# Kernel optimization log

Hardware: AMD Instinct MI355X
Metric: run time of the kernel (lower is better)

Reference implementation:

```python
import jax, jax.numpy as jnp
from jax import lax
import numpy as np

FEA = 256
NHEADS = 8
GROUPS = 32
SCALE = 1.0 / np.sqrt(FEA // NHEADS)  # 1/sqrt(qkv_dim//nheads)


def conv2d(x, w, b=None, pad=0, groups=1):
    out = lax.conv_general_dilated(
        x, w, (1, 1), [(pad, pad), (pad, pad)],
        dimension_numbers=("NCHW", "OIHW", "NCHW"),
        feature_group_count=groups)
    return out if b is None else out + b[None, :, None, None]


def group_norm(x, w, b, groups=GROUPS, eps=1e-5):
    B, C, H, W = x.shape
    xg = x.reshape(B, groups, C // groups, H, W)
    m = xg.mean(axis=(2, 3, 4), keepdims=True)
    v = xg.var(axis=(2, 3, 4), keepdims=True)
    xg = (xg - m) * lax.rsqrt(v + eps)
    return xg.reshape(B, C, H, W) * w[None, :, None, None] + b[None, :, None, None]


def l2norm(x, eps=1e-12):  # F.normalize over channel dim
    n = jnp.sqrt(jnp.sum(x * x, axis=1, keepdims=True))
    return x / jnp.maximum(n, eps)


def attn_op(q, k, v):
    b, c, xf, yf = q.shape
    sp = lambda t: t.reshape(b, NHEADS, c // NHEADS, xf * yf)
    q, k, v = sp(q), sp(k), sp(v)
    sim = jnp.einsum("bhjn,bhkn->bhjk", q, k) * SCALE  # channel attention, [b,h,c/h,c/h]
    sim = jax.nn.softmax(sim, axis=-1)
    out = jnp.einsum("bhjk,bhkn->bhjn", sim, v)
    return out.reshape(b, c, xf, yf)


def freqca(x, gn_w, gn_b, dw_w, pw_w, pw_b, ao_w, ao_b, f1_w, f2_w, f3_w, f3_b):
    H, W = x.shape[-2:]
    x = group_norm(x, gn_w, gn_b)
    qkv = conv2d(conv2d(x, dw_w, pad=1, groups=FEA), pw_w, pw_b)  # depthwise 3x3 then 1x1 -> 3*qkv_dim
    q, k, v = jnp.split(qkv, 3, axis=1)
    q, k, v = l2norm(q), l2norm(k), l2norm(v)
    qf = jnp.fft.rfft2(q, axes=(-2, -1), norm="ortho")
    kf = jnp.fft.rfft2(k, axes=(-2, -1), norm="ortho")
    vf = jnp.fft.rfft2(v, axes=(-2, -1), norm="ortho")
    amp = attn_op(jnp.abs(qf), jnp.abs(kf), jnp.abs(vf))
    phas = attn_op(jnp.angle(qf), jnp.angle(kf), jnp.angle(vf))
    out_c = amp * jnp.cos(phas) + 1j * (amp * jnp.sin(phas))  # torch.polar
    out = jnp.fft.irfft2(out_c, s=(H, W), axes=(-2, -1), norm="ortho")
    attn = conv2d(out, ao_w, ao_b) + x  # attn_res is Identity (fea_dim == dim_out)
    h = jax.nn.silu(conv2d(attn, f1_w, pad=1))
    h = conv2d(h, f2_w, pad=1)
    h = conv2d(h, f3_w, f3_b)
    return h + attn  # DropPath in eval mode = identity


def setup_inputs() -> dict:
    key = jax.random.key(0)
    ks = jax.random.split(key, 12)
    B, C, H, W = 8, FEA, 128, 128
    s = 0.02
    return {
        "x": jax.random.normal(ks[0], (B, C, H, W), jnp.float32),
        "gn_w": jnp.ones((C,), jnp.float32),
        "gn_b": jnp.zeros((C,), jnp.float32),
        "dw_w": jax.random.normal(ks[1], (C, 1, 3, 3), jnp.float32) * s,
        "pw_w": jax.random.normal(ks[2], (3 * C, C, 1, 1), jnp.float32) * s,
        "pw_b": jnp.zeros((3 * C,), jnp.float32),
        "ao_w": jax.random.normal(ks[3], (C, C, 1, 1), jnp.float32) * s,
        "ao_b": jnp.zeros((C,), jnp.float32),
        "f1_w": jax.random.normal(ks[4], (2 * C, C, 3, 3), jnp.float32) * s,
        "f2_w": jax.random.normal(ks[5], (C, 2 * C, 3, 3), jnp.float32) * s,
        "f3_w": jax.random.normal(ks[6], (C, C, 1, 1), jnp.float32) * s,
        "f3_b": jnp.zeros((C,), jnp.float32),
    }


def reference(x, gn_w, gn_b, dw_w, pw_w, pw_b, ao_w, ao_b, f1_w, f2_w, f3_w, f3_b):
    return freqca(x, gn_w, gn_b, dw_w, pw_w, pw_b, ao_w, ao_b, f1_w, f2_w, f3_w, f3_b)
```

## Files before the change

kernel.cpp:

```cpp
#include <hip/hip_runtime.h>
#include <hip/hip_bf16.h>
#include <math.h>


#define TWO_PI_D 6.283185307179586476925286766559
#define ATTN_SCALE 0.17677669529663687f

typedef __attribute__((ext_vector_type(8))) short short8;
typedef __attribute__((ext_vector_type(4))) short short4v;
typedef __attribute__((ext_vector_type(4))) float f32x4;
typedef _Float16 half8v __attribute__((ext_vector_type(8)));

__device__ inline short f2bf(float f) {
    __hip_bfloat16 h = __float2bfloat16(f);
    return *reinterpret_cast<short*>(&h);
}
__device__ inline unsigned short h_bits(_Float16 h) {
    union { _Float16 h; unsigned short u; } c; c.h = h; return c.u;
}

__global__ __launch_bounds__(256) void groupnorm_kernel(
    const float* __restrict__ x, const float* __restrict__ gw,
    const float* __restrict__ gb, float* __restrict__ out, int b0)
{
    int t = threadIdx.x;
    int lb = blockIdx.x >> 5;
    int g  = blockIdx.x & 31;
    size_t src = ((size_t)(b0 + lb) * 32 + g) * 131072;
    size_t dst = (size_t)blockIdx.x * 131072;
    const float* xp = x + src;
    double s = 0.0, ss = 0.0;
    for (int i = t; i < 131072; i += 256) { double v = xp[i]; s += v; ss += v*v; }
    __shared__ double rs[256], rss[256];
    rs[t] = s; rss[t] = ss;
    __syncthreads();
    for (int k = 128; k > 0; k >>= 1) {
        if (t < k) { rs[t] += rs[t+k]; rss[t] += rss[t+k]; }
        __syncthreads();
    }
    __shared__ float smean, sinv;
    if (t == 0) {
        double mean = rs[0] * (1.0/131072.0);
        double var  = rss[0] * (1.0/131072.0) - mean*mean;
        smean = (float)mean;
        sinv  = (float)(1.0 / sqrt(var + 1e-5));
    }
    __syncthreads();
    float mean = smean, inv = sinv;
    for (int i = t; i < 131072; i += 256) {
        int c = (g << 3) + (i >> 14);
        out[dst + i] = (xp[i] - mean) * inv * gw[c] + gb[c];
    }
}

__global__ __launch_bounds__(256) void dwconv_kernel(
    const float* __restrict__ in, const float* __restrict__ w, float* __restrict__ out)
{
    int t = threadIdx.x;
    int bc = blockIdx.x >> 6;
    int y  = ((blockIdx.x & 63) << 1) + (t >> 7);
    int x  = t & 127;
    int c  = bc & 255;
    const float* wp = w + c*9;
    const float* ip = in + ((size_t)bc << 14);
    float acc = 0.f;
    #pragma unroll
    for (int dy = 0; dy < 3; dy++) {
        int yy = y + dy - 1;
        if (yy < 0 || yy > 127) continue;
        const float* row = ip + (yy << 7);
        #pragma unroll
        for (int dx = 0; dx < 3; dx++) {
            int xx = x + dx - 1;
            if (xx >= 0 && xx <= 127) acc += wp[dy*3+dx] * row[xx];
        }
    }
    out[((size_t)bc << 14) + (y << 7) + x] = acc;
}

__global__ __launch_bounds__(256) void wcvtpw_kernel(
    const float* __restrict__ w, _Float16* __restrict__ whi,
    _Float16* __restrict__ wlo, int total)
{
    int i = blockIdx.x * 256 + threadIdx.x;
    if (i >= total) return;
    float v = w[i];
    _Float16 h = (_Float16)v;
    _Float16 l = (_Float16)(v - (float)h);
    whi[i] = h; wlo[i] = l;
}

__global__ __launch_bounds__(256) void twcvt_kernel(
    _Float16* __restrict__ twh, _Float16* __restrict__ twl)
{
    int i = blockIdx.x * 256 + threadIdx.x;
    if (i >= 20480) return;
    int bin = i >> 7, w = i & 127;
    double v = 0.0;
    if (bin < 65) v = cos(TWO_PI_D * ((bin * w) & 127) / 128.0) * 0.0078125;
    else if (bin < 130) v = -sin(TWO_PI_D * (((bin - 65) * w) & 127) / 128.0) * 0.0078125;
    _Float16 h = (_Float16)v;
    twh[i] = h;
    twl[i] = (_Float16)((float)v - (float)h);
}

__global__ __launch_bounds__(256) void convpw_kernel(
    const float* __restrict__ in, const _Float16* __restrict__ whi,
    const _Float16* __restrict__ wlo, const float* __restrict__ bias,
    float* __restrict__ out)
{
    int y      = blockIdx.x;
    int coBase = blockIdx.y << 7;
    int lb     = blockIdx.z;
    int t = threadIdx.x;
    int lane = t & 63;
    int wave = t >> 6;
    int wm = (wave >> 1) << 6;
    int wn = (wave & 1) << 6;
    int lr = lane & 15;
    int kg = (lane >> 4) << 3;

    __shared__ _Float16 Ah[128][40], Al[128][40];
    __shared__ _Float16 Bh[128][40], Bl[128][40];

    f32x4 acc[4][4];
    #pragma unroll
    for (int i = 0; i < 4; i++)
        #pragma unroll
        for (int j = 0; j < 4; j++) acc[i][j] = (f32x4){0.f, 0.f, 0.f, 0.f};

    const float* inrow = in + (((size_t)lb * 256) << 14) + (y << 7);
    for (int ci0 = 0; ci0 < 256; ci0 += 32) {
        __syncthreads();
        #pragma unroll
        for (int u = 0; u < 2; u++) {
            int ii = t + (u << 8);
            int co = ii >> 2, cg = ii & 3;
            *(half8v*)&Ah[co][cg << 3] =
                *(const half8v*)&whi[(size_t)(coBase + co) * 256 + ci0 + (cg << 3)];
            *(half8v*)&Al[co][cg << 3] =
                *(const half8v*)&wlo[(size_t)(coBase + co) * 256 + ci0 + (cg << 3)];
        }
        for (int i = t; i < 2048; i += 256) {
            int px = i & 127, chp = i >> 7;
            int ci = ci0 + (chp << 1);
            float v0 = inrow[((size_t)ci << 14) + px];
            float v1 = inrow[((size_t)(ci + 1) << 14) + px];
            _Float16 h0 = (_Float16)v0, h1 = (_Float16)v1;
            _Float16 l0 = (_Float16)(v0 - (float)h0);
            _Float16 l1 = (_Float16)(v1 - (float)h1);
            unsigned uh = (unsigned)h_bits(h0) | ((unsigned)h_bits(h1) << 16);
            unsigned ul = (unsigned)h_bits(l0) | ((unsigned)h_bits(l1) << 16);
            *(unsigned*)&Bh[px][chp << 1] = uh;
            *(unsigned*)&Bl[px][chp << 1] = ul;
        }
        __syncthreads();
        half8v ah[4], al[4], bh4[4], bl4[4];
        #pragma unroll
        for (int i = 0; i < 4; i++) {
            ah[i] = *(const half8v*)&Ah[wm + i*16 + lr][kg];
            al[i] = *(const half8v*)&Al[wm + i*16 + lr][kg];
        }
        #pragma unroll
        for (int j = 0; j < 4; j++) {
            bh4[j] = *(const half8v*)&Bh[wn + j*16 + lr][kg];
            bl4[j] = *(const half8v*)&Bl[wn + j*16 + lr][kg];
        }
        #pragma unroll
        for (int i = 0; i < 4; i++)
            #pragma unroll
            for (int j = 0; j < 4; j++) {
                acc[i][j] = __builtin_amdgcn_mfma_f32_16x16x32_f16(
                    ah[i], bh4[j], acc[i][j], 0, 0, 0);
                acc[i][j] = __builtin_amdgcn_mfma_f32_16x16x32_f16(
                    ah[i], bl4[j], acc[i][j], 0, 0, 0);
                acc[i][j] = __builtin_amdgcn_mfma_f32_16x16x32_f16(
                    al[i], bh4[j], acc[i][j], 0, 0, 0);
            }
    }

    int pBase = y << 7;
    int mr = (lane >> 4) << 2;
    #pragma unroll
    for (int i = 0; i < 4; i++) {
        int co0 = coBase + wm + i*16 + mr;
        #pragma unroll
        for (int j = 0; j < 4; j++) {
            int px = pBase + wn + j*16 + lr;
            #pragma unroll
            for (int r = 0; r < 4; r++) {
                out[(((size_t)(lb*768 + co0 + r)) << 14) + px] =
                    acc[i][j][r] + bias[co0 + r];
            }
        }
    }
}

__global__ __launch_bounds__(256) void l2inv_kernel(
    const float* __restrict__ qkv, float* __restrict__ invn)
{
    int p  = ((blockIdx.x & 63) << 8) + threadIdx.x;
    int bT = blockIdx.x >> 6;
    int lb = bT / 3, T = bT - 3*lb;
    const float* base = qkv + (((size_t)(lb*768 + T*256)) << 14) + p;
    double ss = 0.0;
    for (int c = 0; c < 256; c++) { double v = base[(size_t)c << 14]; ss += v*v; }
    invn[((size_t)bT << 14) + p] = 1.f / fmaxf((float)sqrt(ss), 1e-12f);
}

__global__ __launch_bounds__(256) void fftrow_mfma_kernel(
    const float* __restrict__ qkv, const float* __restrict__ invn,
    const _Float16* __restrict__ twh, const _Float16* __restrict__ twl,
    float* __restrict__ rre, float* __restrict__ rim, int chunkBase)
{
    int loc = blockIdx.x;
    int gp  = chunkBase + loc;
    int t = threadIdx.x;
    int lane = t & 63;
    int wave = t >> 6;
    int wm  = (wave >> 1) << 6;
    int wnn = (wave & 1) * 80;
    int lr = lane & 15;
    int kq = (lane >> 4) << 3;

    __shared__ _Float16 Xh[128][68], Xl[128][68];

    int lb = gp / 768, chn = gp - lb*768, T = chn >> 8;
    const float4* src = (const float4*)(qkv + ((size_t)gp << 14));
    const float4* ivp = (const float4*)(invn + (((size_t)(lb*3 + T)) << 14));

    f32x4 acc[4][5];
    #pragma unroll
    for (int i = 0; i < 4; i++)
        #pragma unroll
        for (int j = 0; j < 5; j++) acc[i][j] = (f32x4){0.f, 0.f, 0.f, 0.f};

    for (int half = 0; half < 2; half++) {
        __syncthreads();
        for (int i = t; i < 2048; i += 256) {
            int r = i >> 4, q4 = i & 15;
            int gi = (r << 5) + (half << 4) + q4;
            float4 v = src[gi], w = ivp[gi];
            v.x *= w.x; v.y *= w.y; v.z *= w.z; v.w *= w.w;
            int cl = q4 << 2;
            _Float16 h0 = (_Float16)v.x, h1 = (_Float16)v.y;
            _Float16 h2 = (_Float16)v.z, h3 = (_Float16)v.w;
            Xh[r][cl+0] = h0; Xh[r][cl+1] = h1; Xh[r][cl+2] = h2; Xh[r][cl+3] = h3;
            Xl[r][cl+0] = (_Float16)(v.x - (float)h0);
            Xl[r][cl+1] = (_Float16)(v.y - (float)h1);
            Xl[r][cl+2] = (_Float16)(v.z - (float)h2);
            Xl[r][cl+3] = (_Float16)(v.w - (float)h3);
        }
        __syncthreads();
        #pragma unroll
        for (int ks = 0; ks < 2; ks++) {
            int k0 = (ks << 5) + kq;
            int kg = (half << 6) + k0;
            half8v ah[4], al[4], bh[5], bl[5];
            #pragma unroll
            for (int i = 0; i < 4; i++) {
                ah[i] = *(const half8v*)&Xh[wm + i*16 + lr][k0];
                al[i] = *(const half8v*)&Xl[wm + i*16 + lr][k0];
            }
            #pragma unroll
            for (int j = 0; j < 5; j++) {
                int bin = wnn + j*16 + lr;
                bh[j] = *(const half8v*)&twh[(size_t)bin * 128 + kg];
                bl[j] = *(const half8v*)&twl[(size_t)bin * 128 + kg];
            }
            #pragma unroll
            for (int i = 0; i < 4; i++)
                #pragma unroll
                for (int j = 0; j < 5; j++) {
                    acc[i][j] = __builtin_amdgcn_mfma_f32_16x16x32_f16(
                        ah[i], bh[j], acc[i][j], 0, 0, 0);
                    acc[i][j] = __builtin_amdgcn_mfma_f32_16x16x32_f16(
                        al[i], bh[j], acc[i][j], 0, 0, 0);
                    acc[i][j] = __builtin_amdgcn_mfma_f32_16x16x32_f16(
                        ah[i], bl[j], acc[i][j], 0, 0, 0);
                }
        }
    }

    int mr = (lane >> 4) << 2;
    #pragma unroll
    for (int i = 0; i < 4; i++) {
        #pragma unroll
        for (int j = 0; j < 5; j++) {
            int bin = wnn + j*16 + lr;
            if (bin < 130) {
                float* dst = (bin < 65) ? rre : rim;
                int bb = (bin < 65) ? bin : bin - 65;
                #pragma unroll
                for (int r = 0; r < 4; r++) {
                    int row = wm + i*16 + mr + r;
                    dst[((size_t)loc*128 + row)*65 + bb] = acc[i][j][r];
                }
            }
        }
    }
}

__global__ __launch_bounds__(256) void fft_col_kernel(
    const float* __restrict__ rre, const float* __restrict__ rim,
    float* __restrict__ spec, int chunkBase, size_t slotStride)
{
    int kb  = blockIdx.x * 13;
    int loc = blockIdx.y;
    int gp  = chunkBase + loc;
    int t   = threadIdx.x;
    __shared__ float zr[128][14], zi[128][14];
    __shared__ float gr[8][16][14], gi[8][16][14];
    __shared__ float ct[128], st[128];
    if (t < 128) { double s, c; sincos(TWO_PI_D * t / 128.0, &s, &c);
                   st[t] = (float)s; ct[t] = (float)c; }
    for (int i = t; i < 1664; i += 256) {
        int r = i / 13, k = i - r*13;
        size_t si = ((size_t)loc*128 + r)*65 + kb + k;
        zr[r][k] = rre[si];
        zi[r][k] = rim[si];
    }
    __syncthreads();
    for (int i = t; i < 1664; i += 256) {
        int kx = i % 13, rm = i / 13;
        int r0 = rm >> 4, m = rm & 15;
        int step = (m << 3) & 127;
        float gre = 0.f, gim = 0.f;
        int idx = 0;
        for (int r1 = 0; r1 < 16; r1++) {
            float cc = ct[idx], sn = st[idx];
            float a = zr[(r1 << 3) + r0][kx], b = zi[(r1 << 3) + r0][kx];
            gre += a*cc + b*sn;
            gim += b*cc - a*sn;
            idx = (idx + step) & 127;
        }
        gr[r0][m][kx] = gre;
        gi[r0][m][kx] = gim;
    }
    __syncthreads();
    int lb = gp / 768; int chn = gp - lb*768;
    int T = chn >> 8;  int c = chn & 255;
    float* aD = spec + (size_t)(2*T)   * slotStride + ((size_t)(lb*256 + c))*8320;
    float* pD = spec + (size_t)(2*T+1) * slotStride + ((size_t)(lb*256 + c))*8320;
    for (int i = t; i < 1664; i += 256) {
        int kx = i % 13, k1 = i / 13;
        int m = k1 & 15;
        float re = 0.f, im = 0.f;
        int idx = 0;
        for (int r0 = 0; r0 < 8; r0++) {
            float cc = ct[idx], sn = st[idx];
            float a = gr[r0][m][kx], b = gi[r0][m][kx];
            re += a*cc + b*sn;
            im += b*cc - a*sn;
            idx = (idx + k1) & 127;
        }
        int kxv = kb + kx;
        if ((k1 == 0 || k1 == 64) && (kxv == 0 || kxv == 64)) im = 0.f;
        int oi = k1*65 + kxv;
        aD[oi] = sqrtf(re*re + im*im);
        pD[oi] = atan2f(im, re);
    }
}

__global__ __launch_bounds__(256) void attn_sim_kernel(
    const float* __restrict__ qA, const float* __restrict__ kA,
    float* __restrict__ simpart)
{
    int sp = blockIdx.x;
    int bh = blockIdx.y;
    int lb = bh >> 3, h = bh & 7;
    int t = threadIdx.x;
    __shared__ float qs[32][132], ks[32][132];
    const float* qb = qA + ((size_t)(lb*256 + h*32)) * 8320;
    const float* kb = kA + ((size_t)(lb*256 + h*32)) * 8320;
    float acc[4] = {0.f, 0.f, 0.f, 0.f};
    int j0 = t >> 5;
    int kq = t & 31;
    for (int sub = 0; sub < 4; sub++) {
        int n0 = sp*520 + sub*130;
        __syncthreads();
        for (int i = t; i < 4160; i += 256) {
            int j = i / 130, nn = i - j*130;
            qs[j][nn] = qb[(size_t)j*8320 + n0 + nn];
            ks[j][nn] = kb[(size_t)j*8320 + n0 + nn];
        }
        __syncthreads();
        for (int nn = 0; nn < 128; nn += 4) {
            float4 kv = *(const float4*)&ks[kq][nn];
            #pragma unroll
            for (int e = 0; e < 4; e++) {
                float4 qv = *(const float4*)&qs[j0 + e*8][nn];
                acc[e] += qv.x*kv.x + qv.y*kv.y + qv.z*kv.z + qv.w*kv.w;
            }
        }
        {
            float2 kv = *(const float2*)&ks[kq][128];
            #pragma unroll
            for (int e = 0; e < 4; e++) {
                float2 qv = *(const float2*)&qs[j0 + e*8][128];
                acc[e] += qv.x*kv.x + qv.y*kv.y;
            }
        }
    }
    float* dst = simpart + ((size_t)bh*16 + sp) * 1024;
    dst[t]       = acc[0];
    dst[t + 256] = acc[1];
    dst[t + 512] = acc[2];
    dst[t + 768] = acc[3];
}

__global__ __launch_bounds__(256) void attn_out_kernel(
    const float* __restrict__ simpart, const float* __restrict__ vA,
    float* __restrict__ outA)
{
    int nb = blockIdx.x << 8;
    int bh = blockIdx.y;
    int lb = bh >> 3, h = bh & 7;
    int t = threadIdx.x;
    __shared__ float sim[32][32];
    for (int e = t; e < 1024; e += 256) {
        float s = 0.f;
        const float* pp = simpart + (size_t)bh*16384 + e;
        #pragma unroll
        for (int sp = 0; sp < 16; sp++) s += pp[sp*1024];
        sim[e >> 5][e & 31] = s * ATTN_SCALE;
    }
    __syncthreads();
    if (t < 32) {
        float m = -1e30f;
        for (int k = 0; k < 32; k++) m = fmaxf(m, sim[t][k]);
        float s = 0.f;
        for (int k = 0; k < 32; k++) s += expf(sim[t][k] - m);
        float inv = 1.f / s;
        for (int k = 0; k < 32; k++) sim[t][k] = expf(sim[t][k] - m) * inv;
    }
    __syncthreads();
    int n = nb + t;
    if (n >= 8320) return;
    const float* vb = vA + ((size_t)(lb*256 + h*32)) * 8320 + n;
    float vv[32];
    #pragma unroll
    for (int k = 0; k < 32; k++) vv[k] = vb[(size_t)k * 8320];
    float* ob = outA + ((size_t)(lb*256 + h*32)) * 8320 + n;
    for (int j = 0; j < 32; j++) {
        float o = 0.f;
        #pragma unroll
        for (int k = 0; k < 32; k++) o += sim[j][k] * vv[k];
        ob[(size_t)j * 8320] = o;
    }
}

__global__ __launch_bounds__(256) void ifft_col_kernel(
    const float* __restrict__ ampo, const float* __restrict__ pho,
    float* __restrict__ tre, float* __restrict__ tim)
{
    int kb    = blockIdx.x * 13;
    int plane = blockIdx.y;
    int t     = threadIdx.x;
    __shared__ float zr[128][14], zi[128][14];
    __shared__ float gr[8][16][14], gi[8][16][14];
    __shared__ float ct[128], st[128];
    if (t < 128) { double s, c; sincos(TWO_PI_D * t / 128.0, &s, &c);
                   st[t] = (float)s; ct[t] = (float)c; }
    const float* ab = ampo + (size_t)plane * 8320;
    const float* pb = pho  + (size_t)plane * 8320;
    for (int i = t; i < 1664; i += 256) {
        int k1 = i / 13, k = i - k1*13;
        float a = ab[k1*65 + kb + k];
        float p = pb[k1*65 + kb + k];
        float sp, cp; sincosf(p, &sp, &cp);
        zr[k1][k] = a * cp;
        zi[k1][k] = a * sp;
    }
    __syncthreads();
    for (int i = t; i < 1664; i += 256) {
        int kx = i % 13, rm = i / 13;
        int r0 = rm >> 4, m = rm & 15;
        int step = (m << 3) & 127;
        float gre = 0.f, gim = 0.f;
        int idx = 0;
        for (int r1 = 0; r1 < 16; r1++) {
            float cc = ct[idx], sn = st[idx];
            float a = zr[(r1 << 3) + r0][kx], b = zi[(r1 << 3) + r0][kx];
            gre += a*cc - b*sn;
            gim += a*sn + b*cc;
            idx = (idx + step) & 127;
        }
        gr[r0][m][kx] = gre;
        gi[r0][m][kx] = gim;
    }
    __syncthreads();
    for (int i = t; i < 1664; i += 256) {
        int kx = i % 13, y = i / 13;
        int m = y & 15;
        float re = 0.f, im = 0.f;
        int idx = 0;
        for (int r0 = 0; r0 < 8; r0++) {
            float cc = ct[idx], sn = st[idx];
            float a = gr[r0][m][kx], b = gi[r0][m][kx];
            re += a*cc - b*sn;
            im += a*sn + b*cc;
            idx = (idx + y) & 127;
        }
        size_t oi = ((size_t)plane*128 + y)*65 + kb + kx;
        tre[oi] = re;
        tim[oi] = im;
    }
}

__global__ __launch_bounds__(256) void ifft_row_kernel(
    const float* __restrict__ tre, const float* __restrict__ tim,
    float* __restrict__ spat)
{
    int rc    = blockIdx.x;
    int plane = blockIdx.y;
    int t     = threadIdx.x;
    __shared__ float tr[16][66], ti[16][66];
    __shared__ float ct[128], st[128];
    if (t < 128) { double s, c; sincos(TWO_PI_D * t / 128.0, &s, &c);
                   st[t] = (float)s; ct[t] = (float)c; }
    for (int i = t; i < 1040; i += 256) {
        int r = i / 65, k = i - r*65;
        size_t si = ((size_t)plane*128 + rc*16 + r)*65 + k;
        float sc = (k >= 1 && k < 64) ? 2.f : 1.f;
        tr[r][k] = tre[si] * sc;
        ti[r][k] = tim[si] * sc;
    }
    __syncthreads();
    for (int oo = t; oo < 260; oo += 256) {
        int x = oo % 65, rq = oo / 65;
        int r0i = rq << 2;
        float C0 = tr[r0i+0][0], C1 = tr[r0i+1][0], C2 = tr[r0i+2][0], C3 = tr[r0i+3][0];
        float S0 = 0.f, S1 = 0.f, S2 = 0.f, S3 = 0.f;
        int m = x;
        for (int k = 1; k <= 64; k++) {
            float cc = ct[m], sn = st[m];
            C0 += tr[r0i+0][k]*cc; S0 += ti[r0i+0][k]*sn;
            C1 += tr[r0i+1][k]*cc; S1 += ti[r0i+1][k]*sn;
            C2 += tr[r0i+2][k]*cc; S2 += ti[r0i+2][k]*sn;
            C3 += tr[r0i+3][k]*cc; S3 += ti[r0i+3][k]*sn;
            m = (m + x) & 127;
        }
        size_t ob = ((size_t)plane << 14) + ((rc*16 + r0i) << 7);
        spat[ob + x]       = (C0 - S0)*0.0078125f;
        spat[ob + 128 + x] = (C1 - S1)*0.0078125f;
        spat[ob + 256 + x] = (C2 - S2)*0.0078125f;
        spat[ob + 384 + x] = (C3 - S3)*0.0078125f;
        if (x >= 1 && x <= 63) {
            int xm = 128 - x;
            spat[ob + xm]       = (C0 + S0)*0.0078125f;
            spat[ob + 128 + xm] = (C1 + S1)*0.0078125f;
            spat[ob + 256 + xm] = (C2 + S2)*0.0078125f;
            spat[ob + 384 + xm] = (C3 + S3)*0.0078125f;
        }
    }
}

__global__ __launch_bounds__(256) void wcvt_kernel(
    const float* __restrict__ w, short* __restrict__ wbf,
    int Cout, int Cin, int RR)
{
    int i = blockIdx.x * 256 + threadIdx.x;
    int total = Cout * Cin * RR;
    if (i >= total) return;
    int rr = i % RR;
    int ci = (i / RR) % Cin;
    int co = i / (RR * Cin);
    wbf[((size_t)rr * Cout + co) * Cin + ci] = f2bf(w[i]);
}

__global__ __launch_bounds__(256) void convmf2_kernel(
    const float* __restrict__ in, const short* __restrict__ wbf,
    const float* __restrict__ bias, const float* __restrict__ res,
    float* __restrict__ out, short* __restrict__ out_t,
    int Cin, int Cout, int act, int in_b0, int res_b0, int out_b0)
{
    int y      = blockIdx.x;
    int coBase = blockIdx.y << 7;
    int lb = blockIdx.z;
    int t = threadIdx.x;
    int lane = t & 63;
    int wave = t >> 6;
    int wm = (wave >> 1) << 6;
    int wn = (wave & 1) << 6;

    __shared__ short As[128][40];
    __shared__ short Bs[128][40];

    f32x4 acc[4][4];
    #pragma unroll
    for (int i = 0; i < 4; i++)
        #pragma unroll
        for (int j = 0; j < 4; j++) acc[i][j] = (f32x4){0.f, 0.f, 0.f, 0.f};

    const size_t inb = ((size_t)(in_b0 + lb) * Cin) << 14;
    int lr = lane & 15;
    int kg = (lane >> 4) << 3;

    const float* inrow = in + inb + (y << 7);
    const short* wslice = wbf + (size_t)coBase * Cin;
    for (int ci0 = 0; ci0 < Cin; ci0 += 32) {
        __syncthreads();
        #pragma unroll
        for (int u = 0; u < 2; u++) {
            int ii = t + (u << 8);
            int co = ii >> 2, cg = ii & 3;
            *(short8*)&As[co][cg << 3] =
                *(const short8*)&wslice[(size_t)co * Cin + ci0 + (cg << 3)];
        }
        for (int i = t; i < 2048; i += 256) {
            int px = i & 127, chp = i >> 7;
            int ci = ci0 + (chp << 1);
            float v0 = inrow[((size_t)ci << 14) + px];
            float v1 = inrow[((size_t)(ci + 1) << 14) + px];
            unsigned u2 = (unsigned)(unsigned short)f2bf(v0)
                        | ((unsigned)(unsigned short)f2bf(v1) << 16);
            *(unsigned*)&Bs[px][chp << 1] = u2;
        }
        __syncthreads();
        short8 af[4], bf[4];
        #pragma unroll
        for (int i = 0; i < 4; i++)
            af[i] = *(const short8*)&As[wm + i*16 + lr][kg];
        #pragma unroll
        for (int j = 0; j < 4; j++)
            bf[j] = *(const short8*)&Bs[wn + j*16 + lr][kg];
        #pragma unroll
        for (int i = 0; i < 4; i++)
            #pragma unroll
            for (int j = 0; j < 4; j++)
                acc[i][j] = __builtin_amdgcn_mfma_f32_16x16x32_bf16(
                    af[i], bf[j], acc[i][j], 0, 0, 0);
    }

    int pBase = y << 7;
    int mr = (lane >> 4) << 2;
    #pragma unroll
    for (int i = 0; i < 4; i++) {
        int co0 = coBase + wm + i*16 + mr;
        #pragma unroll
        for (int j = 0; j < 4; j++) {
            int px = pBase + wn + j*16 + lr;
            float v[4];
            #pragma unroll
            for (int r = 0; r < 4; r++) {
                float vv = acc[i][j][r] + (bias ? bias[co0 + r] : 0.f);
                if (act == 1) vv = vv / (1.f + expf(-vv));
                if (res) vv += res[(((size_t)(res_b0 + lb) * Cout + co0 + r) << 14) + px];
                v[r] = vv;
            }
            if (out) {
                #pragma unroll
                for (int r = 0; r < 4; r++)
                    out[(((size_t)(out_b0 + lb) * Cout + co0 + r) << 14) + px] = v[r];
            }
            if (out_t) {
                short4v s4 = { f2bf(v[0]), f2bf(v[1]), f2bf(v[2]), f2bf(v[3]) };
                *(short4v*)&out_t[((size_t)(lb*16384 + px)) * Cout + co0] = s4;
            }
        }
    }
}

template<int R>
__global__ __launch_bounds__(256) void convmf3_kernel(
    const short* __restrict__ in_t, const short* __restrict__ wbf,
    const float* __restrict__ bias, const float* __restrict__ res,
    float* __restrict__ out, short* __restrict__ out_t,
    int Cin, int Cout, int act, int res_b0, int out_b0)
{
    int y      = blockIdx.x;
    int coBase = blockIdx.y << 7;
    int lb = blockIdx.z;
    int t = threadIdx.x;
    int lane = t & 63;
    int wave = t >> 6;
    int wm = (wave >> 1) << 6;
    int wn = (wave & 1) << 6;
    int lr = lane & 15;
    int kg = (lane >> 4) << 3;

    f32x4 acc[4][4];
    #pragma unroll
    for (int i = 0; i < 4; i++)
        #pragma unroll
        for (int j = 0; j < 4; j++) acc[i][j] = (f32x4){0.f, 0.f, 0.f, 0.f};

    const short* inb = in_t + (((size_t)lb << 14)) * Cin;
    const short8 zero8 = {0,0,0,0,0,0,0,0};

    for (int rr = 0; rr < R*R; rr++) {
        int dy = (R == 3) ? (rr / 3) : 0;
        int dx = (R == 3) ? (rr - dy*3) : 0;
        int yy = (R == 3) ? (y + dy - 1) : y;
        if (R == 3 && (yy < 0 || yy > 127)) continue;
        const short* wsl  = wbf + ((size_t)rr * Cout + coBase) * Cin;
        const short* brow = inb + ((size_t)(yy << 7)) * Cin;
        for (int ci0 = 0; ci0 < Cin; ci0 += 32) {
            short8 af[4], bf[4];
            #pragma unroll
            for (int i = 0; i < 4; i++)
                af[i] = *(const short8*)&wsl[(size_t)(wm + i*16 + lr) * Cin + ci0 + kg];
            #pragma unroll
            for (int j = 0; j < 4; j++) {
                int pxl = wn + j*16 + lr;
                int xx = (R == 3) ? (pxl + dx - 1) : pxl;
                if (R == 3 && (xx < 0 || xx > 127)) bf[j] = zero8;
                else bf[j] = *(const short8*)&brow[(size_t)xx * Cin + ci0 + kg];
            }
            #pragma unroll
            for (int i = 0; i < 4; i++)
                #pragma unroll
                for (int j = 0; j < 4; j++)
                    acc[i][j] = __builtin_amdgcn_mfma_f32_16x16x32_bf16(
                        af[i], bf[j], acc[i][j], 0, 0, 0);
        }
    }

    int pBase = y << 7;
    int mr = (lane >> 4) << 2;
    #pragma unroll
    for (int i = 0; i < 4; i++) {
        int co0 = coBase + wm + i*16 + mr;
        #pragma unroll
        for (int j = 0; j < 4; j++) {
            int px = pBase + wn + j*16 + lr;
            float v[4];
            #pragma unroll
            for (int r = 0; r < 4; r++) {
                float vv = acc[i][j][r] + (bias ? bias[co0 + r] : 0.f);
                if (act == 1) vv = vv / (1.f + expf(-vv));
                if (res) vv += res[(((size_t)(res_b0 + lb) * Cout + co0 + r) << 14) + px];
                v[r] = vv;
            }
            if (out) {
                #pragma unroll
                for (int r = 0; r < 4; r++)
                    out[(((size_t)(out_b0 + lb) * Cout + co0 + r) << 14) + px] = v[r];
            }
            if (out_t) {
                short4v s4 = { f2bf(v[0]), f2bf(v[1]), f2bf(v[2]), f2bf(v[3]) };
                *(short4v*)&out_t[((size_t)(lb*16384 + px)) * Cout + co0] = s4;
            }
        }
    }
}

extern "C" void kernel_launch(void* const* d_in, const int* in_sizes, int n_in,
                              void* d_out, int out_size, void* d_ws, size_t ws_size,
                              hipStream_t stream) {
    (void)in_sizes; (void)n_in; (void)out_size;
    const float* x    = (const float*)d_in[0];
    const float* gn_w = (const float*)d_in[1];
    const float* gn_b = (const float*)d_in[2];
    const float* dw_w = (const float*)d_in[3];
    const float* pw_w = (const float*)d_in[4];
    const float* pw_b = (const float*)d_in[5];
    const float* ao_w = (const float*)d_in[6];
    const float* ao_b = (const float*)d_in[7];
    const float* f1_w = (const float*)d_in[8];
    const float* f2_w = (const float*)d_in[9];
    const float* f3_w = (const float*)d_in[10];
    const float* f3_b = (const float*)d_in[11];
    float* outp = (float*)d_out;

    const size_t F_QKV  = 12582912;
    const size_t F_SLOT = 2129920;
    const size_t F_SPEC = 6 * F_SLOT;
    const size_t F_XN   = 4194304;
    const size_t F_E    = 4259840;
    const size_t F_SIMP = 262144;
    const size_t F_TOT  = F_QKV + F_SPEC + F_XN + F_E + F_SIMP;
    const size_t F_WB   = 1462272;

    int NB = 0;
    for (int cand : {8, 4, 2, 1}) {
        if (((size_t)cand * F_TOT + F_WB) * 4 <= ws_size) { NB = cand; break; }
    }
    if (NB == 0) return;

    float* wsf  = (float*)d_ws;
    float* qkv  = wsf;
    short* abuf = (short*)wsf;
    short* h1t  = (short*)(wsf + (size_t)NB * 2097152);
    short* h2t  = (short*)(wsf + (size_t)NB * 6291456);
    float* spec = wsf + (size_t)NB * F_QKV;
    size_t ss   = (size_t)NB * F_SLOT;
    float* tre  = spec + 2*ss;
    float* tim  = spec + 3*ss;
    float* spat = spec + 4*ss;
    float* xn   = spec + 6*ss;
    float* ebuf = xn + (size_t)NB * F_XN;
    float* dw   = ebuf;
    float* rre  = ebuf;
    float* rim  = ebuf + (size_t)NB * 2129920;
    float* simpf = ebuf + (size_t)NB * F_E;
    float* invn  = simpf;
    float* simp  = simpf;
    short* wb    = (short*)(wsf + (size_t)NB * F_TOT);
    short* wb_ao = wb;
    short* wb_f1 = wb + 65536;
    short* wb_f2 = wb + 1245184;
    short* wb_f3 = wb + 2424832;
    _Float16* wb_pw_hi = (_Float16*)(wb + 2490368);
    _Float16* wb_pw_lo = (_Float16*)(wb + 2686976);
    _Float16* wb_tw_hi = (_Float16*)(wb + 2883584);
    _Float16* wb_tw_lo = (_Float16*)(wb + 2904064);

    wcvt_kernel<<<256,  256, 0, stream>>>(ao_w, wb_ao, 256, 256, 1);
    wcvt_kernel<<<4608, 256, 0, stream>>>(f1_w, wb_f1, 512, 256, 9);
    wcvt_kernel<<<4608, 256, 0, stream>>>(f2_w, wb_f2, 256, 512, 9);
    wcvt_kernel<<<256,  256, 0, stream>>>(f3_w, wb_f3, 256, 256, 1);
    wcvtpw_kernel<<<768, 256, 0, stream>>>(pw_w, wb_pw_hi, wb_pw_lo, 196608);
    twcvt_kernel<<<80, 256, 0, stream>>>(wb_tw_hi, wb_tw_lo);

    const int passes = 8 / NB;
    for (int p = 0; p < passes; p++) {
        int b0 = p * NB;
        groupnorm_kernel<<<NB*32, 256, 0, stream>>>(x, gn_w, gn_b, xn, b0);
        dwconv_kernel<<<NB*256*64, 256, 0, stream>>>(xn, dw_w, dw);
        convpw_kernel<<<dim3(128, 6, NB), 256, 0, stream>>>(
            dw, wb_pw_hi, wb_pw_lo, pw_b, qkv);
        l2inv_kernel<<<NB*3*64, 256, 0, stream>>>(qkv, invn);
        for (int chunk = 0; chunk < 3; chunk++) {
            fftrow_mfma_kernel<<<NB*256, 256, 0, stream>>>(
                qkv, invn, wb_tw_hi, wb_tw_lo, rre, rim, chunk*NB*256);
            fft_col_kernel<<<dim3(5, NB*256), 256, 0, stream>>>(
                rre, rim, spec, chunk*NB*256, ss);
        }
        attn_sim_kernel<<<dim3(16, NB*8), 256, 0, stream>>>(spec + 0*ss, spec + 2*ss, simp);
        attn_out_kernel<<<dim3(33, NB*8), 256, 0, stream>>>(simp, spec + 4*ss, spec + 0*ss);
        attn_sim_kernel<<<dim3(16, NB*8), 256, 0, stream>>>(spec + 1*ss, spec + 3*ss, simp);
        attn_out_kernel<<<dim3(33, NB*8), 256, 0, stream>>>(simp, spec + 5*ss, spec + 1*ss);
        ifft_col_kernel<<<dim3(5, NB*256), 256, 0, stream>>>(spec + 0*ss, spec + 1*ss,
                                                             tre, tim);
        ifft_row_kernel<<<dim3(8, NB*256), 256, 0, stream>>>(tre, tim, spat);
        convmf2_kernel<<<dim3(128, 2, NB), 256, 0, stream>>>(
            spat, wb_ao, ao_b, xn, outp, abuf, 256, 256, 0, 0, 0, b0);
        convmf3_kernel<3><<<dim3(128, 4, NB), 256, 0, stream>>>(
            abuf, wb_f1, nullptr, nullptr, nullptr, h1t, 256, 512, 1, 0, 0);
        convmf3_kernel<3><<<dim3(128, 2, NB), 256, 0, stream>>>(
            h1t, wb_f2, nullptr, nullptr, nullptr, h2t, 512, 256, 0, 0, 0);
        convmf3_kernel<1><<<dim3(128, 2, NB), 256, 0, stream>>>(
            h2t, wb_f3, f3_b, outp, outp, nullptr, 256, 256, 0, b0, b0);
    }
}
```

Baseline: 6.460 ms.

## Replace inverse column FFT with split-fp16 MFMA DFT matmul; tile dwconv rows in LDS

The inverse FFT along the column axis is recast as a dense complex DFT matrix multiply (a 256x256 real-expanded twiddle matrix) executed with fp16 MFMA using hi/lo splitting for near-fp32 accuracy, replacing the scalar radix-16x8 shared-memory DFT. A new precompute kernel builds the twiddle matrix once. The depthwise conv now stages its four input rows in shared memory to avoid redundant global loads. The MFMA path does more raw flops than an FFT and relies on three-term split precision, trading arithmetic count for matrix-core throughput.

```diff
diff --git a/kernel.cpp b/kernel.cpp
--- a/kernel.cpp
+++ b/kernel.cpp
@@ -58,24 +58,30 @@
 {
     int t = threadIdx.x;
     int bc = blockIdx.x >> 6;
-    int y  = ((blockIdx.x & 63) << 1) + (t >> 7);
-    int x  = t & 127;
+    int ystrip = (blockIdx.x & 63) << 1;
     int c  = bc & 255;
     const float* wp = w + c*9;
     const float* ip = in + ((size_t)bc << 14);
+    __shared__ float xs[4][128];
+    for (int i = t; i < 512; i += 256) {
+        int rr = i >> 7, xx = i & 127;
+        int yy = ystrip - 1 + rr;
+        xs[rr][xx] = (yy >= 0 && yy < 128) ? ip[(yy << 7) + xx] : 0.f;
+    }
+    __syncthreads();
+    int r0 = t >> 7;
+    int x  = t & 127;
     float acc = 0.f;
     #pragma unroll
     for (int dy = 0; dy < 3; dy++) {
-        int yy = y + dy - 1;
-        if (yy < 0 || yy > 127) continue;
-        const float* row = ip + (yy << 7);
+        const float* row = xs[r0 + dy];
         #pragma unroll
         for (int dx = 0; dx < 3; dx++) {
             int xx = x + dx - 1;
             if (xx >= 0 && xx <= 127) acc += wp[dy*3+dx] * row[xx];
         }
     }
-    out[((size_t)bc << 14) + (y << 7) + x] = acc;
+    out[((size_t)bc << 14) + ((ystrip + r0) << 7) + x] = acc;
 }
 
 __global__ __launch_bounds__(256) void wcvtpw_kernel(
@@ -102,6 +108,24 @@
     _Float16 h = (_Float16)v;
     twh[i] = h;
     twl[i] = (_Float16)((float)v - (float)h);
+}
+
+__global__ __launch_bounds__(256) void micvt_kernel(
+    _Float16* __restrict__ mih, _Float16* __restrict__ mil)
+{
+    int i = blockIdx.x * 256 + threadIdx.x;
+    if (i >= 65536) return;
+    int row = i >> 8, col = i & 255;
+    int k1 = col >> 1, u = col & 1;
+    int yy = row & 127;
+    double ang = TWO_PI_D * ((k1 * yy) & 127) / 128.0;
+    double cc = cos(ang), sn = sin(ang);
+    double v;
+    if (row < 128) v = (u == 0) ? cc : -sn;
+    else           v = (u == 0) ? sn :  cc;
+    _Float16 h = (_Float16)v;
+    mih[i] = h;
+    mil[i] = (_Float16)((float)v - (float)h);
 }
 
 __global__ __launch_bounds__(256) void convpw_kernel(
@@ -450,61 +474,95 @@
     }
 }
 
-__global__ __launch_bounds__(256) void ifft_col_kernel(
+__global__ __launch_bounds__(256) void ifftcol_mfma_kernel(
     const float* __restrict__ ampo, const float* __restrict__ pho,
+    const _Float16* __restrict__ mih, const _Float16* __restrict__ mil,
     float* __restrict__ tre, float* __restrict__ tim)
 {
-    int kb    = blockIdx.x * 13;
-    int plane = blockIdx.y;
-    int t     = threadIdx.x;
-    __shared__ float zr[128][14], zi[128][14];
-    __shared__ float gr[8][16][14], gi[8][16][14];
-    __shared__ float ct[128], st[128];
-    if (t < 128) { double s, c; sincos(TWO_PI_D * t / 128.0, &s, &c);
-                   st[t] = (float)s; ct[t] = (float)c; }
+    int plane = blockIdx.x;
+    int t = threadIdx.x;
+    int lane = t & 63;
+    int wave = t >> 6;
+    int wm = wave << 6;
+    int lr = lane & 15;
+    int kg = (lane >> 4) << 3;
+
+    __shared__ _Float16 Bh[80][72], Bl[80][72];
+
     const float* ab = ampo + (size_t)plane * 8320;
     const float* pb = pho  + (size_t)plane * 8320;
-    for (int i = t; i < 1664; i += 256) {
-        int k1 = i / 13, k = i - k1*13;
-        float a = ab[k1*65 + kb + k];
-        float p = pb[k1*65 + kb + k];
-        float sp, cp; sincosf(p, &sp, &cp);
-        zr[k1][k] = a * cp;
-        zi[k1][k] = a * sp;
-    }
-    __syncthreads();
-    for (int i = t; i < 1664; i += 256) {
-        int kx = i % 13, rm = i / 13;
-        int r0 = rm >> 4, m = rm & 15;
-        int step = (m << 3) & 127;
-        float gre = 0.f, gim = 0.f;
-        int idx = 0;
-        for (int r1 = 0; r1 < 16; r1++) {
-            float cc = ct[idx], sn = st[idx];
-            float a = zr[(r1 << 3) + r0][kx], b = zi[(r1 << 3) + r0][kx];
-            gre += a*cc - b*sn;
-            gim += a*sn + b*cc;
-            idx = (idx + step) & 127;
-        }
-        gr[r0][m][kx] = gre;
-        gi[r0][m][kx] = gim;
-    }
-    __syncthreads();
-    for (int i = t; i < 1664; i += 256) {
-        int kx = i % 13, y = i / 13;
-        int m = y & 15;
-        float re = 0.f, im = 0.f;
-        int idx = 0;
-        for (int r0 = 0; r0 < 8; r0++) {
-            float cc = ct[idx], sn = st[idx];
-            float a = gr[r0][m][kx], b = gi[r0][m][kx];
-            re += a*cc - b*sn;
-            im += a*sn + b*cc;
-            idx = (idx + y) & 127;
-        }
-        size_t oi = ((size_t)plane*128 + y)*65 + kb + kx;
-        tre[oi] = re;
-        tim[oi] = im;
+
+    f32x4 acc[4][5];
+    #pragma unroll
+    for (int i = 0; i < 4; i++)
+        #pragma unroll
+        for (int j = 0; j < 5; j++) acc[i][j] = (f32x4){0.f, 0.f, 0.f, 0.f};
+
+    for (int kc = 0; kc < 4; kc++) {
+        __syncthreads();
+        for (int i = t; i < 2080; i += 256) {
+            int k1l = i / 65, kx = i - k1l*65;
+            int k1 = (kc << 5) + k1l;
+            float a = ab[k1*65 + kx];
+            float p = pb[k1*65 + kx];
+            float sp, cp; sincosf(p, &sp, &cp);
+            float zr = a * cp, zi = a * sp;
+            _Float16 hr = (_Float16)zr, hi = (_Float16)zi;
+            unsigned uh = (unsigned)h_bits(hr) | ((unsigned)h_bits(hi) << 16);
+            unsigned ul = (unsigned)h_bits((_Float16)(zr - (float)hr))
+                        | ((unsigned)h_bits((_Float16)(zi - (float)hi)) << 16);
+            *(unsigned*)&Bh[kx][k1l << 1] = uh;
+            *(unsigned*)&Bl[kx][k1l << 1] = ul;
+        }
+        __syncthreads();
+        #pragma unroll
+        for (int ks = 0; ks < 2; ks++) {
+            int kq = (ks << 5) + kg;
+            int kgl = (kc << 6) + kq;
+            half8v ah[4], al[4], bh[5], bl[5];
+            #pragma unroll
+            for (int i = 0; i < 4; i++) {
+                int row = wm + i*16 + lr;
+                ah[i] = *(const half8v*)&mih[(size_t)row * 256 + kgl];
+                al[i] = *(const half8v*)&mil[(size_t)row * 256 + kgl];
+            }
+            #pragma unroll
+            for (int j = 0; j < 5; j++) {
+                int col = j*16 + lr;
+                bh[j] = *(const half8v*)&Bh[col][kq];
+                bl[j] = *(const half8v*)&Bl[col][kq];
+            }
+            #pragma unroll
+            for (int i = 0; i < 4; i++)
+                #pragma unroll
+                for (int j = 0; j < 5; j++) {
+                    acc[i][j] = __builtin_amdgcn_mfma_f32_16x16x32_f16(
+                        ah[i], bh[j], acc[i][j], 0, 0, 0);
+                    acc[i][j] = __builtin_amdgcn_mfma_f32_16x16x32_f16(
+                        al[i], bh[j], acc[i][j], 0, 0, 0);
+                    acc[i][j] = __builtin_amdgcn_mfma_f32_16x16x32_f16(
+                        ah[i], bl[j], acc[i][j], 0, 0, 0);
+                }
+        }
+    }
+
+    int mr = (lane >> 4) << 2;
+    #pragma unroll
+    for (int i = 0; i < 4; i++) {
+        #pragma unroll
+        for (int j = 0; j < 5; j++) {
+            int col = j*16 + lr;
+            if (col < 65) {
+                #pragma unroll
+                for (int r = 0; r < 4; r++) {
+                    int row = wm + i*16 + mr + r;
+                    if (row < 128)
+                        tre[((size_t)plane*128 + row)*65 + col] = acc[i][j][r];
+                    else
+                        tim[((size_t)plane*128 + (row - 128))*65 + col] = acc[i][j][r];
+                }
+            }
+        }
     }
 }
 
@@ -771,7 +829,7 @@
     const size_t F_E    = 4259840;
     const size_t F_SIMP = 262144;
     const size_t F_TOT  = F_QKV + F_SPEC + F_XN + F_E + F_SIMP;
-    const size_t F_WB   = 1462272;
+    const size_t F_WB   = 1527808;
 
     int NB = 0;
     for (int cand : {8, 4, 2, 1}) {
@@ -806,6 +864,8 @@
     _Float16* wb_pw_lo = (_Float16*)(wb + 2686976);
     _Float16* wb_tw_hi = (_Float16*)(wb + 2883584);
     _Float16* wb_tw_lo = (_Float16*)(wb + 2904064);
+    _Float16* wb_mi_hi = (_Float16*)(wb + 2924544);
+    _Float16* wb_mi_lo = (_Float16*)(wb + 2990080);
 
     wcvt_kernel<<<256,  256, 0, stream>>>(ao_w, wb_ao, 256, 256, 1);
     wcvt_kernel<<<4608, 256, 0, stream>>>(f1_w, wb_f1, 512, 256, 9);
@@ -813,6 +873,7 @@
     wcvt_kernel<<<256,  256, 0, stream>>>(f3_w, wb_f3, 256, 256, 1);
     wcvtpw_kernel<<<768, 256, 0, stream>>>(pw_w, wb_pw_hi, wb_pw_lo, 196608);
     twcvt_kernel<<<80, 256, 0, stream>>>(wb_tw_hi, wb_tw_lo);
+    micvt_kernel<<<256, 256, 0, stream>>>(wb_mi_hi, wb_mi_lo);
 
     const int passes = 8 / NB;
     for (int p = 0; p < passes; p++) {
@@ -832,8 +893,8 @@
         attn_out_kernel<<<dim3(33, NB*8), 256, 0, stream>>>(simp, spec + 4*ss, spec + 0*ss);
         attn_sim_kernel<<<dim3(16, NB*8), 256, 0, stream>>>(spec + 1*ss, spec + 3*ss, simp);
         attn_out_kernel<<<dim3(33, NB*8), 256, 0, stream>>>(simp, spec + 5*ss, spec + 1*ss);
-        ifft_col_kernel<<<dim3(5, NB*256), 256, 0, stream>>>(spec + 0*ss, spec + 1*ss,
-                                                             tre, tim);
+        ifftcol_mfma_kernel<<<NB*256, 256, 0, stream>>>(
+            spec + 0*ss, spec + 1*ss, wb_mi_hi, wb_mi_lo, tre, tim);
         ifft_row_kernel<<<dim3(8, NB*256), 256, 0, stream>>>(tre, tim, spat);
         convmf2_kernel<<<dim3(128, 2, NB), 256, 0, stream>>>(
             spat, wb_ao, ao_b, xn, outp, abuf, 256, 256, 0, 0, 0, b0);
```

Result: faster. 6.333 ms (-2.0%).
